# Performance work log

Hardware: AMD Instinct MI355X
Metric: run time of the kernel (lower is better)

The kernel has to match this reference:

```python
import jax, jax.numpy as jnp
import numpy as np

EPS = 1e-5

def conv(x, w, stride=1, pad=0):
    # x: NCHW, w: OIHW
    return jax.lax.conv_general_dilated(
        x, w, (stride, stride), [(pad, pad), (pad, pad)],
        dimension_numbers=('NCHW', 'OIHW', 'NCHW'))

def bn(x, g, b, m, v):
    scale = (g * jax.lax.rsqrt(v + EPS))[None, :, None, None]
    shift = (b - m * g * jax.lax.rsqrt(v + EPS))[None, :, None, None]
    return x * scale + shift

def dilate3x3(mask):
    # binary dilation == 3x3 max-pool, stride 1, pad 1
    return jax.lax.reduce_window(mask, -jnp.inf, jax.lax.max,
                                 (1, 1, 3, 3), (1, 1, 1, 1),
                                 [(0, 0), (0, 0), (1, 1), (1, 1)])

def setup_inputs() -> dict:
    key = jax.random.key(0)
    ks = jax.random.split(key, 8)
    B, Cin, H, W = 32, 256, 56, 56
    width, Cout = 64, 256
    f32 = jnp.float32
    return {
        'x':       jax.random.normal(ks[0], (B, Cin, H, W), f32),
        'conv1_w': jax.random.normal(ks[1], (width, Cin, 1, 1), f32) * 0.05,
        'conv2_w': jax.random.normal(ks[2], (width, width, 3, 3), f32) * 0.05,
        'conv3_w': jax.random.normal(ks[3], (Cout, width, 1, 1), f32) * 0.05,
        'bn1_g': jnp.ones((width,), f32), 'bn1_b': jnp.zeros((width,), f32),
        'bn1_m': jax.random.normal(ks[4], (width,), f32) * 0.1,
        'bn1_v': jax.random.uniform(ks[4], (width,), f32, 0.5, 1.5),
        'bn2_g': jnp.ones((width,), f32), 'bn2_b': jnp.zeros((width,), f32),
        'bn2_m': jax.random.normal(ks[5], (width,), f32) * 0.1,
        'bn2_v': jax.random.uniform(ks[5], (width,), f32, 0.5, 1.5),
        'bn3_g': jnp.ones((Cout,), f32), 'bn3_b': jnp.zeros((Cout,), f32),
        'bn3_m': jax.random.normal(ks[6], (Cout,), f32) * 0.1,
        'bn3_v': jax.random.uniform(ks[6], (Cout,), f32, 0.5, 1.5),
        'mask_w': jax.random.normal(ks[7], (1, Cin, 1, 1), f32) * 0.05,
        'mask_b': jnp.zeros((1,), f32),
    }

def reference(x, conv1_w, conv2_w, conv3_w,
              bn1_g, bn1_b, bn1_m, bn1_v,
              bn2_g, bn2_b, bn2_m, bn2_v,
              bn3_g, bn3_b, bn3_m, bn3_v,
              mask_w, mask_b):
    identity = x  # stride=1, no downsample
    # --- MaskUnit: 1x1 conv squeeze -> hard binary mask (inference Gumbel) ---
    soft = conv(x, mask_w) + mask_b[None, :, None, None]   # [B,1,H,W]
    mask = (soft >= 0.0).astype(x.dtype)                    # 'std' mask
    mask_dilate = dilate3x3(mask)                           # 'dilate' mask
    # --- sparse bottleneck: compute only on active positions (zero elsewhere) ---
    h = conv(x, conv1_w)                                    # [B,64,H,W]
    h = jax.nn.relu(bn(h, bn1_g, bn1_b, bn1_m, bn1_v)) * mask_dilate
    h = conv(h, conv2_w, stride=1, pad=1)
    h = jax.nn.relu(bn(h, bn2_g, bn2_b, bn2_m, bn2_v)) * mask
    h = conv(h, conv3_w)                                    # [B,256,H,W]
    h = bn(h, bn3_g, bn3_b, bn3_m, bn3_v) * mask            # apply_mask
    out = jax.nn.relu(identity + h)
    return out
```

## Files before the change

kernel.cpp:

```cpp
#include <hip/hip_runtime.h>
#include <hip/hip_bf16.h>


#define BATCH 32
#define CIN   256
#define WIDTH 64
#define COUT  256
#define HH    56
#define WW    56
#define HW    3136
#define EPS   1e-5f
#define XSTR  40
#define H1ROW 7424

typedef __attribute__((ext_vector_type(8))) short bf16x8;
typedef __attribute__((ext_vector_type(4))) float f32x4;

static __device__ __forceinline__ unsigned short f2bf(float f) {
    __hip_bfloat16 h = __float2bfloat16(f);
    return *reinterpret_cast<unsigned short*>(&h);
}

__global__ __launch_bounds__(256) void kw_pack(
    const float* __restrict__ w1, const float* __restrict__ w2,
    const float* __restrict__ w3, __hip_bfloat16* __restrict__ w1p,
    __hip_bfloat16* __restrict__ w2p, __hip_bfloat16* __restrict__ w3q,
    const float* __restrict__ g1, const float* __restrict__ b1,
    const float* __restrict__ m1, const float* __restrict__ v1,
    const float* __restrict__ g2, const float* __restrict__ b2,
    const float* __restrict__ m2, const float* __restrict__ v2,
    const float* __restrict__ g3, const float* __restrict__ b3,
    const float* __restrict__ m3, const float* __restrict__ v3,
    float* __restrict__ tabs)
{
    if (blockIdx.x == 272) {
        for (int t = threadIdx.x; t < 384; t += 256) {
            if (t < 64) {
                float sc = g1[t] * rsqrtf(v1[t] + EPS);
                tabs[t] = sc; tabs[64 + t] = b1[t] - m1[t] * sc;
            } else if (t < 128) {
                int o = t - 64;
                float sc = g2[o] * rsqrtf(v2[o] + EPS);
                tabs[128 + o] = sc; tabs[192 + o] = b2[o] - m2[o] * sc;
            } else {
                int o = t - 128;
                float sc = g3[o] * rsqrtf(v3[o] + EPS);
                tabs[256 + o] = sc; tabs[512 + o] = b3[o] - m3[o] * sc;
            }
        }
        return;
    }
    int idx = blockIdx.x * 256 + threadIdx.x;
    if (idx < 16384) {
        int j = idx & 7, l = (idx >> 3) & 63;
        int mt = (idx >> 9) & 3, kt = idx >> 11;
        int o = mt * 16 + (l & 15);
        int c = kt * 32 + (l >> 4) * 8 + j;
        *reinterpret_cast<unsigned short*>(w1p + idx) = f2bf(w1[o * CIN + c]);
    } else if (idx < 16384 + 36864) {
        int i2 = idx - 16384;
        int j = i2 & 7, l = (i2 >> 3) & 63;
        int mt = (i2 >> 9) & 3, kt = (i2 >> 11) & 1, tap = i2 >> 12;
        int o = mt * 16 + (l & 15);
        int c = kt * 32 + (l >> 4) * 8 + j;
        *reinterpret_cast<unsigned short*>(w2p + i2) =
            f2bf(w2[(o * WIDTH + c) * 9 + tap]);
    } else if (idx < 16384 + 36864 + 16384) {
        int i3 = idx - 16384 - 36864;
        int j = i3 & 7, l = (i3 >> 3) & 63;
        int ot = (i3 >> 9) & 15, kt = i3 >> 13;
        int oc = ot * 16 + (l & 15);
        int c = kt * 32 + (l >> 4) * 8 + j;
        *reinterpret_cast<unsigned short*>(w3q + i3) = f2bf(w3[oc * WIDTH + c]);
    }
}

__global__ __launch_bounds__(256) void k1_mfma(
    const float* __restrict__ x, const __hip_bfloat16* __restrict__ w1p,
    const float* __restrict__ sc1, const float* __restrict__ sh1,
    const float* __restrict__ mw, const float* __restrict__ mb,
    __hip_bfloat16* __restrict__ h1g, float* __restrict__ mask)
{
    __shared__ __align__(16) unsigned short xs[2][64 * XSTR];
    __shared__ __align__(16) float mtab[16][68];

    const int tid = threadIdx.x;
    const int l = tid & 63, w = tid >> 6;
    const int ln = l & 15, lg = l >> 4;
    const int b = blockIdx.y;
    const int px0 = blockIdx.x * 64;
    const float* __restrict__ xb = x + (size_t)b * CIN * HW;
    const bf16x8* __restrict__ w1v = reinterpret_cast<const bf16x8*>(w1p);

    const int chA = tid >> 4;
    const int pxs = (tid & 15) * 4;
    float msum[4] = {0.f, 0.f, 0.f, 0.f};

    auto STAGE = [&](int kt, int bufi) {
        const float* xp = xb + (size_t)(kt * 32 + chA) * HW + px0 + pxs;
        float4 va = *reinterpret_cast<const float4*>(xp);
        float4 vb = *reinterpret_cast<const float4*>(xp + (size_t)16 * HW);
        float mwa = mw[kt * 32 + chA], mwb = mw[kt * 32 + 16 + chA];
        msum[0] += va.x * mwa + vb.x * mwb;
        msum[1] += va.y * mwa + vb.y * mwb;
        msum[2] += va.z * mwa + vb.z * mwb;
        msum[3] += va.w * mwa + vb.w * mwb;
        unsigned base = (unsigned)pxs * XSTR + chA;
        xs[bufi][base + 0 * XSTR] = f2bf(va.x);
        xs[bufi][base + 1 * XSTR] = f2bf(va.y);
        xs[bufi][base + 2 * XSTR] = f2bf(va.z);
        xs[bufi][base + 3 * XSTR] = f2bf(va.w);
        xs[bufi][base + 16 + 0 * XSTR] = f2bf(vb.x);
        xs[bufi][base + 16 + 1 * XSTR] = f2bf(vb.y);
        xs[bufi][base + 16 + 2 * XSTR] = f2bf(vb.z);
        xs[bufi][base + 16 + 3 * XSTR] = f2bf(vb.w);
    };

    f32x4 acc[4];
    #pragma unroll
    for (int m = 0; m < 4; ++m) acc[m] = f32x4{0.f, 0.f, 0.f, 0.f};

    STAGE(0, 0);
    __syncthreads();

    const unsigned fidx = (unsigned)(w * 16 + ln) * XSTR + lg * 8;
    #pragma unroll
    for (int kt = 0; kt < 8; ++kt) {
        const int cur = kt & 1;
        if (kt < 7) STAGE(kt + 1, cur ^ 1);
        bf16x8 bfr = *reinterpret_cast<const bf16x8*>(&xs[cur][fidx]);
        #pragma unroll
        for (int mt = 0; mt < 4; ++mt) {
            bf16x8 a = w1v[(kt * 4 + mt) * 64 + l];
            acc[mt] = __builtin_amdgcn_mfma_f32_16x16x32_bf16(a, bfr, acc[mt], 0, 0, 0);
        }
        __syncthreads();
    }

    *reinterpret_cast<float4*>(&mtab[chA][pxs]) =
        make_float4(msum[0], msum[1], msum[2], msum[3]);
    __syncthreads();
    if (tid < 64) {
        float s = 0.f;
        #pragma unroll
        for (int g = 0; g < 16; ++g) s += mtab[g][tid];
        mask[b * HW + px0 + tid] = (s + mb[0] >= 0.f) ? 1.f : 0.f;
    }

    const int p = px0 + w * 16 + ln;
    const int y = p / 56, xcn = p - y * 56;
    const int pxp = xcn + 1;
    const unsigned key = (unsigned)(pxp & 7) << 3;
    const size_t rowbase = (((size_t)b * 58 + y + 1) * 58 + pxp) * 64;
    #pragma unroll
    for (int mt = 0; mt < 4; ++mt) {
        int ob = mt * 16 + lg * 4;
        ushort4 u;
        u.x = f2bf(fmaxf(acc[mt][0] * sc1[ob + 0] + sh1[ob + 0], 0.f));
        u.y = f2bf(fmaxf(acc[mt][1] * sc1[ob + 1] + sh1[ob + 1], 0.f));
        u.z = f2bf(fmaxf(acc[mt][2] * sc1[ob + 2] + sh1[ob + 2], 0.f));
        u.w = f2bf(fmaxf(acc[mt][3] * sc1[ob + 3] + sh1[ob + 3], 0.f));
        *reinterpret_cast<ushort4*>(h1g + rowbase + (ob ^ key)) = u;
    }
}

__global__ __launch_bounds__(256) void k2_mfma(
    const __hip_bfloat16* __restrict__ h1g,
    const __hip_bfloat16* __restrict__ w2p,
    const float* __restrict__ sc2, const float* __restrict__ sh2,
    const float* __restrict__ mask, __hip_bfloat16* __restrict__ h2)
{
    __shared__ __align__(16) char smem[30720];

    const int tid = threadIdx.x;
    const int l = tid & 63, w = tid >> 6;
    const int b = blockIdx.y;
    const int yr0 = blockIdx.x * 2;
    const int yrow = yr0 + (w & 1);
    const int mh = w >> 1;
    const int ln = l & 15, lg = l >> 4;

    {
        const char* src = (const char*)h1g + ((size_t)b * 58 + yr0) * H1ROW;
        #pragma unroll
        for (int t = 0; t < 8; ++t) {
            int c = t * 4 + w;
            if (c < 29) {
                __builtin_amdgcn_global_load_lds(
                    (const __attribute__((address_space(1))) void*)(src + c * 1024 + l * 16),
                    (__attribute__((address_space(3))) void*)(smem + c * 1024),
                    16, 0, 0);
            }
        }
    }

    const bf16x8* __restrict__ w2v = reinterpret_cast<const bf16x8*>(w2p);

    f32x4 acc[2][4];
    #pragma unroll
    for (int i = 0; i < 2; ++i)
        #pragma unroll
        for (int j = 0; j < 4; ++j) acc[i][j] = f32x4{0.f, 0.f, 0.f, 0.f};

    __syncthreads();

    if (tid < 232) {
        const int pr = tid / 58;
        const int pc = tid - pr * 58;
        const int gr = yr0 + pr;
        bool zero;
        if (gr == 0 || gr == 57 || pc == 0 || pc == 57) {
            zero = true;
        } else {
            const int y = gr - 1, xc = pc - 1;
            float mx = 0.f;
            #pragma unroll
            for (int dy = -1; dy <= 1; ++dy)
                #pragma unroll
                for (int dx = -1; dx <= 1; ++dx) {
                    int yy = y + dy, xx = xc + dx;
                    if (yy >= 0 && yy < HH && xx >= 0 && xx < WW)
                        mx = fmaxf(mx, mask[b * HW + yy * WW + xx]);
                }
            zero = (mx < 0.5f);
        }
        if (zero) {
            uint4* q = reinterpret_cast<uint4*>(smem + pr * H1ROW + pc * 128);
            uint4 zz = make_uint4(0u, 0u, 0u, 0u);
            #pragma unroll
            for (int k = 0; k < 8; ++k) q[k] = zz;
        }
    }
    __syncthreads();

    #pragma unroll
    for (int dy = 0; dy < 3; ++dy) {
        const int lr = (w & 1) + dy;
        #pragma unroll
        for (int dx = 0; dx < 3; ++dx) {
            const int tap = dy * 3 + dx;
            #pragma unroll
            for (int kt = 0; kt < 2; ++kt) {
                bf16x8 a0 = w2v[((tap * 2 + kt) * 4 + mh * 2 + 0) * 64 + l];
                bf16x8 a1 = w2v[((tap * 2 + kt) * 4 + mh * 2 + 1) * 64 + l];
                bf16x8 bf[4];
                #pragma unroll
                for (int nt = 0; nt < 4; ++nt) {
                    int colp = nt * 16 + ln + dx;
                    unsigned off = (unsigned)lr * H1ROW + (unsigned)colp * 128
                                 + (((unsigned)(kt * 64 + lg * 16))
                                    ^ (((unsigned)colp & 7u) << 4));
                    bf[nt] = *reinterpret_cast<const bf16x8*>(smem + off);
                }
                #pragma unroll
                for (int nt = 0; nt < 4; ++nt) {
                    acc[0][nt] = __builtin_amdgcn_mfma_f32_16x16x32_bf16(
                        a0, bf[nt], acc[0][nt], 0, 0, 0);
                    acc[1][nt] = __builtin_amdgcn_mfma_f32_16x16x32_bf16(
                        a1, bf[nt], acc[1][nt], 0, 0, 0);
                }
            }
        }
    }

    #pragma unroll
    for (int nt = 0; nt < 4; ++nt) {
        int xc = nt * 16 + ln;
        if (xc < WW) {
            int p = yrow * WW + xc;
            float mkv = mask[b * HW + p];
            #pragma unroll
            for (int mi = 0; mi < 2; ++mi) {
                int ob = (mh * 2 + mi) * 16 + lg * 4;
                ushort4 u;
                u.x = f2bf(fmaxf(acc[mi][nt][0] * sc2[ob + 0] + sh2[ob + 0], 0.f) * mkv);
                u.y = f2bf(fmaxf(acc[mi][nt][1] * sc2[ob + 1] + sh2[ob + 1], 0.f) * mkv);
                u.z = f2bf(fmaxf(acc[mi][nt][2] * sc2[ob + 2] + sh2[ob + 2], 0.f) * mkv);
                u.w = f2bf(fmaxf(acc[mi][nt][3] * sc2[ob + 3] + sh2[ob + 3], 0.f) * mkv);
                *reinterpret_cast<ushort4*>(h2 + ((size_t)b * HW + p) * 64 + ob) = u;
            }
        }
    }
}

__global__ __launch_bounds__(256) void k3_mfma(
    const __hip_bfloat16* __restrict__ h2, const __hip_bfloat16* __restrict__ w3q,
    const float* __restrict__ sc3, const float* __restrict__ sh3,
    const float* __restrict__ x, const float* __restrict__ mask,
    float* __restrict__ out)
{
    const int tid = threadIdx.x;
    const int l = tid & 63, w = tid >> 6;
    const int ln = l & 15, lg = l >> 4;
    const int b = blockIdx.y;
    const int yr = blockIdx.x;
    const int z = blockIdx.z;

    const bf16x8* __restrict__ h2v = reinterpret_cast<const bf16x8*>(h2)
                                   + ((size_t)b * HW + yr * WW) * 8;
    const bf16x8* __restrict__ w3v = reinterpret_cast<const bf16x8*>(w3q);

    float4 mk4[4];
    #pragma unroll
    for (int pt = 0; pt < 4; ++pt) {
        int pxb = pt * 16 + lg * 4;
        mk4[pt] = (pxb < WW)
            ? *reinterpret_cast<const float4*>(&mask[(size_t)b * HW + yr * WW + pxb])
            : make_float4(0.f, 0.f, 0.f, 0.f);
    }
    float4 xv[2][4];
    #pragma unroll
    for (int ot = 0; ot < 2; ++ot) {
        const int oc = w * 64 + z * 32 + ot * 16 + ln;
        const size_t rbase = ((size_t)b * COUT + oc) * HW + yr * WW;
        #pragma unroll
        for (int pt = 0; pt < 4; ++pt) {
            int pxb = pt * 16 + lg * 4;
            if (pxb < WW)
                xv[ot][pt] = *reinterpret_cast<const float4*>(&x[rbase + pxb]);
        }
    }

    f32x4 acc[4][2];
    #pragma unroll
    for (int p = 0; p < 4; ++p)
        #pragma unroll
        for (int o = 0; o < 2; ++o) acc[p][o] = f32x4{0.f, 0.f, 0.f, 0.f};

    #pragma unroll
    for (int kt = 0; kt < 2; ++kt) {
        bf16x8 af[4];
        #pragma unroll
        for (int pt = 0; pt < 4; ++pt)
            af[pt] = h2v[(pt * 16 + ln) * 8 + kt * 4 + lg];
        #pragma unroll
        for (int ot = 0; ot < 2; ++ot) {
            bf16x8 bw = w3v[(kt * 16 + w * 4 + z * 2 + ot) * 64 + l];
            #pragma unroll
            for (int pt = 0; pt < 4; ++pt)
                acc[pt][ot] = __builtin_amdgcn_mfma_f32_16x16x32_bf16(
                    af[pt], bw, acc[pt][ot], 0, 0, 0);
        }
    }

    #pragma unroll
    for (int ot = 0; ot < 2; ++ot) {
        const int oc = w * 64 + z * 32 + ot * 16 + ln;
        const float sc = sc3[oc], sh = sh3[oc];
        const size_t rbase = ((size_t)b * COUT + oc) * HW + yr * WW;
        #pragma unroll
        for (int pt = 0; pt < 4; ++pt) {
            int pxb = pt * 16 + lg * 4;
            if (pxb < WW) {
                float4 o4;
                o4.x = fmaxf(xv[ot][pt].x + (acc[pt][ot][0] * sc + sh) * mk4[pt].x, 0.f);
                o4.y = fmaxf(xv[ot][pt].y + (acc[pt][ot][1] * sc + sh) * mk4[pt].y, 0.f);
                o4.z = fmaxf(xv[ot][pt].z + (acc[pt][ot][2] * sc + sh) * mk4[pt].z, 0.f);
                o4.w = fmaxf(xv[ot][pt].w + (acc[pt][ot][3] * sc + sh) * mk4[pt].w, 0.f);
                *reinterpret_cast<float4*>(&out[rbase + pxb]) = o4;
            }
        }
    }
}

extern "C" void kernel_launch(void* const* d_in, const int* in_sizes, int n_in,
                              void* d_out, int out_size, void* d_ws, size_t ws_size,
                              hipStream_t stream)
{
    const float* x  = (const float*)d_in[0];
    const float* w1 = (const float*)d_in[1];
    const float* w2 = (const float*)d_in[2];
    const float* w3 = (const float*)d_in[3];
    const float* g1 = (const float*)d_in[4];
    const float* b1 = (const float*)d_in[5];
    const float* m1 = (const float*)d_in[6];
    const float* v1 = (const float*)d_in[7];
    const float* g2 = (const float*)d_in[8];
    const float* b2 = (const float*)d_in[9];
    const float* m2 = (const float*)d_in[10];
    const float* v2 = (const float*)d_in[11];
    const float* g3 = (const float*)d_in[12];
    const float* b3 = (const float*)d_in[13];
    const float* m3 = (const float*)d_in[14];
    const float* v3 = (const float*)d_in[15];
    const float* mw = (const float*)d_in[16];
    const float* mb = (const float*)d_in[17];
    float* outp = (float*)d_out;

    char* p = (char*)d_ws;
    __hip_bfloat16* h1g = (__hip_bfloat16*)p;  p += (size_t)BATCH * 3364 * 64 * 2;
    __hip_bfloat16* h2  = (__hip_bfloat16*)p;  p += (size_t)BATCH * HW * 64 * 2;
    float* mask = (float*)p;                   p += (size_t)BATCH * HW * 4;
    __hip_bfloat16* w1p = (__hip_bfloat16*)p;  p += 16384 * 2;
    __hip_bfloat16* w2p = (__hip_bfloat16*)p;  p += 36864 * 2;
    __hip_bfloat16* w3q = (__hip_bfloat16*)p;  p += 16384 * 2;
    float* tabs = (float*)p;
    float* sc1 = tabs;       float* sh1 = tabs + 64;
    float* sc2 = tabs + 128; float* sh2 = tabs + 192;
    float* sc3 = tabs + 256; float* sh3 = tabs + 512;

    kw_pack<<<dim3(273), dim3(256), 0, stream>>>(w1, w2, w3, w1p, w2p, w3q,
                                                 g1, b1, m1, v1, g2, b2, m2, v2,
                                                 g3, b3, m3, v3, tabs);

    k1_mfma<<<dim3(49, BATCH), dim3(256), 0, stream>>>(x, w1p, sc1, sh1, mw, mb,
                                                       h1g, mask);

    k2_mfma<<<dim3(HH / 2, BATCH), dim3(256), 0, stream>>>(h1g, w2p, sc2, sh2,
                                                           mask, h2);

    k3_mfma<<<dim3(HH, BATCH, 2), dim3(256), 0, stream>>>(h2, w3q, sc3, sh3,
                                                          x, mask, outp);
}
```

Measured before the change: 98.75 us.

## Stage conv3 output through LDS for coalesced residual epilogue over wider pixel bands

k3 now processes a 224-pixel band (4 image rows) per block instead of one 56-pixel row, removing the wasted padded MFMA tiles. The BN3+mask result is written as bf16 into a shared-memory tile, then re-read with a thread mapping that streams x and out in contiguous 32-byte chunks per channel row. This targets better coalescing and less tail waste in the bandwidth-heavy residual epilogue. In exchange it rounds the conv3 branch to bf16 before the residual add, uses about 59KB of LDS and 112 accumulator registers, which lowers occupancy.

```diff
diff --git a/kernel.cpp b/kernel.cpp
--- a/kernel.cpp
+++ b/kernel.cpp
@@ -289,77 +289,84 @@
     const float* __restrict__ x, const float* __restrict__ mask,
     float* __restrict__ out)
 {
+    __shared__ __align__(16) unsigned short h3s[128][232];
+
     const int tid = threadIdx.x;
     const int l = tid & 63, w = tid >> 6;
     const int ln = l & 15, lg = l >> 4;
     const int b = blockIdx.y;
-    const int yr = blockIdx.x;
+    const int band0 = blockIdx.x * 224;
     const int z = blockIdx.z;
 
     const bf16x8* __restrict__ h2v = reinterpret_cast<const bf16x8*>(h2)
-                                   + ((size_t)b * HW + yr * WW) * 8;
+                                   + ((size_t)b * HW + band0) * 8;
     const bf16x8* __restrict__ w3v = reinterpret_cast<const bf16x8*>(w3q);
 
-    float4 mk4[4];
-    #pragma unroll
-    for (int pt = 0; pt < 4; ++pt) {
-        int pxb = pt * 16 + lg * 4;
-        mk4[pt] = (pxb < WW)
-            ? *reinterpret_cast<const float4*>(&mask[(size_t)b * HW + yr * WW + pxb])
-            : make_float4(0.f, 0.f, 0.f, 0.f);
-    }
-    float4 xv[2][4];
+    f32x4 acc[14][2];
+    #pragma unroll
+    for (int p = 0; p < 14; ++p)
+        #pragma unroll
+        for (int o = 0; o < 2; ++o) acc[p][o] = f32x4{0.f, 0.f, 0.f, 0.f};
+
+    #pragma unroll
+    for (int kt = 0; kt < 2; ++kt) {
+        bf16x8 bw0 = w3v[(kt * 16 + w * 4 + z * 2 + 0) * 64 + l];
+        bf16x8 bw1 = w3v[(kt * 16 + w * 4 + z * 2 + 1) * 64 + l];
+        #pragma unroll
+        for (int pt = 0; pt < 14; ++pt) {
+            bf16x8 af = h2v[(pt * 16 + ln) * 8 + kt * 4 + lg];
+            acc[pt][0] = __builtin_amdgcn_mfma_f32_16x16x32_bf16(
+                af, bw0, acc[pt][0], 0, 0, 0);
+            acc[pt][1] = __builtin_amdgcn_mfma_f32_16x16x32_bf16(
+                af, bw1, acc[pt][1], 0, 0, 0);
+        }
+    }
+
+    float scv[2], shv[2];
     #pragma unroll
     for (int ot = 0; ot < 2; ++ot) {
         const int oc = w * 64 + z * 32 + ot * 16 + ln;
-        const size_t rbase = ((size_t)b * COUT + oc) * HW + yr * WW;
-        #pragma unroll
-        for (int pt = 0; pt < 4; ++pt) {
-            int pxb = pt * 16 + lg * 4;
-            if (pxb < WW)
-                xv[ot][pt] = *reinterpret_cast<const float4*>(&x[rbase + pxb]);
-        }
-    }
-
-    f32x4 acc[4][2];
-    #pragma unroll
-    for (int p = 0; p < 4; ++p)
-        #pragma unroll
-        for (int o = 0; o < 2; ++o) acc[p][o] = f32x4{0.f, 0.f, 0.f, 0.f};
-
-    #pragma unroll
-    for (int kt = 0; kt < 2; ++kt) {
-        bf16x8 af[4];
-        #pragma unroll
-        for (int pt = 0; pt < 4; ++pt)
-            af[pt] = h2v[(pt * 16 + ln) * 8 + kt * 4 + lg];
+        scv[ot] = sc3[oc]; shv[ot] = sh3[oc];
+    }
+    #pragma unroll
+    for (int pt = 0; pt < 14; ++pt) {
+        const float4 mk = *reinterpret_cast<const float4*>(
+            &mask[(size_t)b * HW + band0 + pt * 16 + lg * 4]);
         #pragma unroll
         for (int ot = 0; ot < 2; ++ot) {
-            bf16x8 bw = w3v[(kt * 16 + w * 4 + z * 2 + ot) * 64 + l];
-            #pragma unroll
-            for (int pt = 0; pt < 4; ++pt)
-                acc[pt][ot] = __builtin_amdgcn_mfma_f32_16x16x32_bf16(
-                    af[pt], bw, acc[pt][ot], 0, 0, 0);
-        }
-    }
-
-    #pragma unroll
-    for (int ot = 0; ot < 2; ++ot) {
-        const int oc = w * 64 + z * 32 + ot * 16 + ln;
-        const float sc = sc3[oc], sh = sh3[oc];
-        const size_t rbase = ((size_t)b * COUT + oc) * HW + yr * WW;
-        #pragma unroll
-        for (int pt = 0; pt < 4; ++pt) {
-            int pxb = pt * 16 + lg * 4;
-            if (pxb < WW) {
-                float4 o4;
-                o4.x = fmaxf(xv[ot][pt].x + (acc[pt][ot][0] * sc + sh) * mk4[pt].x, 0.f);
-                o4.y = fmaxf(xv[ot][pt].y + (acc[pt][ot][1] * sc + sh) * mk4[pt].y, 0.f);
-                o4.z = fmaxf(xv[ot][pt].z + (acc[pt][ot][2] * sc + sh) * mk4[pt].z, 0.f);
-                o4.w = fmaxf(xv[ot][pt].w + (acc[pt][ot][3] * sc + sh) * mk4[pt].w, 0.f);
-                *reinterpret_cast<float4*>(&out[rbase + pxb]) = o4;
-            }
-        }
+            const int rl = w * 32 + ot * 16 + ln;
+            ushort4 u;
+            u.x = f2bf((acc[pt][ot][0] * scv[ot] + shv[ot]) * mk.x);
+            u.y = f2bf((acc[pt][ot][1] * scv[ot] + shv[ot]) * mk.y);
+            u.z = f2bf((acc[pt][ot][2] * scv[ot] + shv[ot]) * mk.z);
+            u.w = f2bf((acc[pt][ot][3] * scv[ot] + shv[ot]) * mk.w);
+            *reinterpret_cast<ushort4*>(&h3s[rl][pt * 16 + lg * 4]) = u;
+        }
+    }
+    __syncthreads();
+
+    #pragma unroll
+    for (int k = 0; k < 14; ++k) {
+        const int g = tid + 256 * k;
+        const int r = g / 28;
+        const int f = g - r * 28;
+        const int oc = ((r >> 5) << 6) + z * 32 + (r & 31);
+        const int px = f * 8;
+        const size_t idx = ((size_t)b * COUT + oc) * HW + band0 + px;
+        const uint4 hv = *reinterpret_cast<const uint4*>(&h3s[r][px]);
+        const float4 xa = *reinterpret_cast<const float4*>(&x[idx]);
+        const float4 xb = *reinterpret_cast<const float4*>(&x[idx + 4]);
+        float4 oa, ob;
+        oa.x = fmaxf(xa.x + __uint_as_float(hv.x << 16), 0.f);
+        oa.y = fmaxf(xa.y + __uint_as_float(hv.x & 0xffff0000u), 0.f);
+        oa.z = fmaxf(xa.z + __uint_as_float(hv.y << 16), 0.f);
+        oa.w = fmaxf(xa.w + __uint_as_float(hv.y & 0xffff0000u), 0.f);
+        ob.x = fmaxf(xb.x + __uint_as_float(hv.z << 16), 0.f);
+        ob.y = fmaxf(xb.y + __uint_as_float(hv.z & 0xffff0000u), 0.f);
+        ob.z = fmaxf(xb.z + __uint_as_float(hv.w << 16), 0.f);
+        ob.w = fmaxf(xb.w + __uint_as_float(hv.w & 0xffff0000u), 0.f);
+        *reinterpret_cast<float4*>(&out[idx]) = oa;
+        *reinterpret_cast<float4*>(&out[idx + 4]) = ob;
     }
 }
 
@@ -409,6 +416,6 @@
     k2_mfma<<<dim3(HH / 2, BATCH), dim3(256), 0, stream>>>(h1g, w2p, sc2, sh2,
                                                            mask, h2);
 
-    k3_mfma<<<dim3(HH, BATCH, 2), dim3(256), 0, stream>>>(h2, w3q, sc3, sh3,
+    k3_mfma<<<dim3(14, BATCH, 2), dim3(256), 0, stream>>>(h2, w3q, sc3, sh3,
                                                           x, mask, outp);
 }
```

Result: no change. 99.26 us (+0.5%).
